# Performance work log

Hardware: AMD Instinct MI355X
Metric: run time of the kernel (lower is better)

## Reference

```python
import jax, jax.numpy as jnp
import numpy as np

B, T, D = 128, 80, 2048
H = 512          # visual_rnn_size; bidirectional output = 2H = 1024
K = 512          # visual_kernel_num
WS = (2, 3, 4, 5)
MAP_IN, MAP_OUT = 2 * H + len(WS) * K + D, 2048
EPS_BN = 1e-5


def _gru_dir(x, Wih, Whh, bih, bhh, reverse):
    """Single-direction PyTorch-convention GRU over [B,T,D] -> [B,T,H]."""
    Hh = Whh.shape[1]
    pre = jnp.einsum('btd,gd->btg', x, Wih) + bih  # [B,T,3H], gates (r,z,n)
    if reverse:
        pre = pre[:, ::-1]

    def step(h, p):
        gh = h @ Whh.T + bhh
        r = jax.nn.sigmoid(p[..., :Hh] + gh[..., :Hh])
        z = jax.nn.sigmoid(p[..., Hh:2 * Hh] + gh[..., Hh:2 * Hh])
        n = jnp.tanh(p[..., 2 * Hh:] + r * gh[..., 2 * Hh:])
        hn = (1.0 - z) * n + z * h
        return hn, hn

    h0 = jnp.zeros((x.shape[0], Hh), x.dtype)
    _, hs = jax.lax.scan(step, h0, jnp.swapaxes(pre, 0, 1))
    hs = jnp.swapaxes(hs, 0, 1)
    return hs[:, ::-1] if reverse else hs


def setup_inputs() -> dict:
    key = jax.random.key(0)
    ks = iter(jax.random.split(key, 40))
    f32 = jnp.float32

    videos = jax.random.normal(next(ks), (B, T, D), f32)
    videos_origin = jax.random.normal(next(ks), (B, D), f32)
    lengths = jax.random.randint(next(ks), (B,), 1, T + 1, jnp.int32)
    vidoes_mask = (jnp.arange(T)[None, :] < lengths[:, None]).astype(f32)
    gru_text_out = jax.random.normal(next(ks), (B, 1024), f32)

    def lin(k, fan_in, shape):
        return jax.random.normal(k, shape, f32) * (1.0 / np.sqrt(fan_in))

    inp = dict(videos=videos, videos_origin=videos_origin, lengths=lengths,
               vidoes_mask=vidoes_mask, gru_text_out=gru_text_out)
    # bidirectional GRU params (PyTorch layout: [3H, in])
    inp['Wih_f'] = lin(next(ks), D, (3 * H, D)); inp['Whh_f'] = lin(next(ks), H, (3 * H, H))
    inp['bih_f'] = jnp.zeros((3 * H,), f32);     inp['bhh_f'] = jnp.zeros((3 * H,), f32)
    inp['Wih_b'] = lin(next(ks), D, (3 * H, D)); inp['Whh_b'] = lin(next(ks), H, (3 * H, H))
    inp['bih_b'] = jnp.zeros((3 * H,), f32);     inp['bhh_b'] = jnp.zeros((3 * H,), f32)
    # attention layer
    inp['att_W1'] = lin(next(ks), 2 * H, (2 * H, 2 * H)); inp['att_b1'] = jnp.zeros((2 * H,), f32)
    inp['att_W2'] = lin(next(ks), 2 * H, (1, 2 * H));     inp['att_b2'] = jnp.zeros((1,), f32)
    # multi-window convs: kernel [K, 1, w, 2H]
    for w in WS:
        inp[f'conv_w{w}'] = lin(next(ks), w * 2 * H, (K, 1, w, 2 * H))
        inp[f'conv_b{w}'] = jnp.zeros((K,), f32)
    # visual mapping + BN
    inp['map_W'] = lin(next(ks), MAP_IN, (MAP_OUT, MAP_IN)); inp['map_b'] = jnp.zeros((MAP_OUT,), f32)
    inp['bn_gamma'] = jnp.ones((MAP_OUT,), f32); inp['bn_beta'] = jnp.zeros((MAP_OUT,), f32)
    return inp


def reference(videos, videos_origin, lengths, vidoes_mask, gru_text_out,
              Wih_f, Whh_f, bih_f, bhh_f, Wih_b, Whh_b, bih_b, bhh_b,
              att_W1, att_b1, att_W2, att_b2,
              conv_w2, conv_b2, conv_w3, conv_b3, conv_w4, conv_b4, conv_w5, conv_b5,
              map_W, map_b, bn_gamma, bn_beta):
    # bidirectional GRU -> [B,T,2H]
    gru = jnp.concatenate([
        _gru_dir(videos, Wih_f, Whh_f, bih_f, bhh_f, False),
        _gru_dir(videos, Wih_b, Whh_b, bih_b, bhh_b, True)], axis=-1)
    # attention (softmax over size-1 dim, as in the original)
    att = jax.nn.softmax(jnp.tanh(gru @ att_W1.T + att_b1) @ att_W2.T + att_b2, axis=-1)
    H2 = gru * att
    # ragged masked mean over valid frames (replaces per-sample python loop)
    len_f = lengths.astype(videos.dtype)
    mean_gru = jnp.sum(H2 * vidoes_mask[:, :, None], axis=1) / len_f[:, None]
    # multi-window CNN over masked sequence
    masked = (H2 * vidoes_mask[:, :, None])[:, None, :, :]  # [B,1,T,2H]
    convs = [(2, conv_w2, conv_b2), (3, conv_w3, conv_b3), (4, conv_w4, conv_b4), (5, conv_w5, conv_b5)]
    outs = []
    for (w, cw, cb) in convs:
        c = jax.lax.conv_general_dilated(masked, cw, (1, 1), [(w - 1, w - 1), (0, 0)],
                                         dimension_numbers=('NCHW', 'OIHW', 'NCHW'))
        c = jax.nn.relu(c + cb.reshape(1, -1, 1, 1))[..., 0]  # [B,K,T+w-1]
        outs.append(jnp.max(c, axis=2))
    con = jnp.concatenate(outs, axis=1)  # [B, 4K]
    # concate == 'full'
    feat = jnp.concatenate([mean_gru, con, videos_origin], axis=1) @ map_W.T + map_b
    # BatchNorm1d in eval mode (running_mean=0, running_var=1)
    feat = feat / jnp.sqrt(jnp.asarray(1.0 + EPS_BN, feat.dtype)) * bn_gamma + bn_beta
    # l2norm
    return feat / jnp.sqrt(jnp.sum(feat * feat, axis=1, keepdims=True))
```

## Files before the change

kernel.cpp:

```cpp
#include <hip/hip_runtime.h>
#include <hip/hip_bf16.h>


#define T_SEQ 80

typedef __attribute__((ext_vector_type(8))) short short8;
typedef __attribute__((ext_vector_type(4))) float floatx4;

__device__ __forceinline__ float bf2f(unsigned short s) {
    union { unsigned int u; float f; } c; c.u = ((unsigned int)s) << 16; return c.f;
}
__device__ __forceinline__ unsigned short f2bf(float f) {
    union { float f; unsigned int u; } c; c.f = f;
    unsigned int u = c.u;
    u += 0x7fffu + ((u >> 16) & 1u);
    return (unsigned short)(u >> 16);
}
__device__ __forceinline__ void gld16(const unsigned short* g, unsigned short* lds_uniform) {
    __builtin_amdgcn_global_load_lds(
        (const __attribute__((address_space(1))) void*)g,
        (__attribute__((address_space(3))) void*)lds_uniform, 16, 0, 0);
}
__device__ __forceinline__ void stage8_f32(const float* __restrict__ src, unsigned short* __restrict__ dst) {
    float4 a = *(const float4*)src;
    float4 b = *(const float4*)(src + 4);
    short8 v;
    v[0] = (short)f2bf(a.x); v[1] = (short)f2bf(a.y); v[2] = (short)f2bf(a.z); v[3] = (short)f2bf(a.w);
    v[4] = (short)f2bf(b.x); v[5] = (short)f2bf(b.y); v[6] = (short)f2bf(b.z); v[7] = (short)f2bf(b.w);
    *(short8*)dst = v;
}

__global__ __launch_bounds__(256) void k_f2b(
    const float* __restrict__ src, unsigned short* __restrict__ dst, int n8)
{
    int e = blockIdx.x * 256 + threadIdx.x;
    if (e >= n8) return;
    float4 a = ((const float4*)src)[e * 2];
    float4 b = ((const float4*)src)[e * 2 + 1];
    short8 v;
    v[0] = (short)f2bf(a.x); v[1] = (short)f2bf(a.y); v[2] = (short)f2bf(a.z); v[3] = (short)f2bf(a.w);
    v[4] = (short)f2bf(b.x); v[5] = (short)f2bf(b.y); v[6] = (short)f2bf(b.z); v[7] = (short)f2bf(b.w);
    *(short8*)(dst + e * 8) = v;
}

template<int AF32, int BF32, int OUTBF>
__global__ __launch_bounds__(256) void gemm_mfma(
    const void* __restrict__ Av, long a_base, int a_rpb, long a_bstride, int a_rstride,
    const void* __restrict__ B1v, const void* __restrict__ B2v,
    int n_split, int b_mod, long b_sa, long b_sb,
    const float* __restrict__ bias1, const float* __restrict__ bias2, int has_bias,
    void* __restrict__ Cout, long out_dsplit, long ldc,
    int kchunk, long zout)
{
    __shared__ __align__(16) unsigned short As[128 * 32];
    __shared__ __align__(16) unsigned short Bs[128 * 32];
    const int tid = threadIdx.x, wave = tid >> 6, lane = tid & 63;
    const int m0 = blockIdx.y * 128, n0 = blockIdx.x * 128;
    const long kbeg = (long)blockIdx.z * kchunk;

    const int c0 = wave * 64 + lane, c1 = 256 + c0;
    const int rA0 = c0 >> 2, pA0 = c0 & 3, rA1 = c1 >> 2, pA1 = c1 & 3;
    const int am0 = m0 + rA0, am1 = m0 + rA1;
    const long aoff0 = a_base + (long)(am0 / a_rpb) * a_bstride + (long)(am0 % a_rpb) * a_rstride + pA0 * 8 + kbeg;
    const long aoff1 = a_base + (long)(am1 / a_rpb) * a_bstride + (long)(am1 % a_rpb) * a_rstride + pA1 * 8 + kbeg;

    const int bn0 = n0 + rA0, bn1 = n0 + rA1;
    const int bd0 = (bn0 >= n_split), bd1 = (bn1 >= n_split);
    const int br0 = bn0 - (bd0 ? n_split : 0), br1 = bn1 - (bd1 ? n_split : 0);
    const long boff0 = (long)(br0 % b_mod) * b_sa + (long)(br0 / b_mod) * b_sb + pA0 * 8 + kbeg;
    const long boff1 = (long)(br1 % b_mod) * b_sa + (long)(br1 / b_mod) * b_sb + pA1 * 8 + kbeg;
    const void* Bp0 = bd0 ? B2v : B1v;
    const void* Bp1 = bd1 ? B2v : B1v;

    const int frow = lane & 15, fq = lane >> 4;
    const int wm = (wave >> 1) * 64, wn = (wave & 1) * 64;

    floatx4 acc[4][4];
    #pragma unroll
    for (int i = 0; i < 4; ++i)
        #pragma unroll
        for (int j = 0; j < 4; ++j) acc[i][j] = (floatx4)0.f;

    for (int k0 = 0; k0 < kchunk; k0 += 32) {
        if (AF32) {
            stage8_f32((const float*)Av + aoff0 + k0, As + c0 * 8);
            stage8_f32((const float*)Av + aoff1 + k0, As + c1 * 8);
        } else {
            gld16((const unsigned short*)Av + aoff0 + k0, As + (wave * 64) * 8);
            gld16((const unsigned short*)Av + aoff1 + k0, As + (256 + wave * 64) * 8);
        }
        if (BF32) {
            stage8_f32((const float*)Bp0 + boff0 + k0, Bs + c0 * 8);
            stage8_f32((const float*)Bp1 + boff1 + k0, Bs + c1 * 8);
        } else {
            gld16((const unsigned short*)Bp0 + boff0 + k0, Bs + (wave * 64) * 8);
            gld16((const unsigned short*)Bp1 + boff1 + k0, Bs + (256 + wave * 64) * 8);
        }
        __syncthreads();
        short8 af[4], bf[4];
        #pragma unroll
        for (int i = 0; i < 4; ++i) {
            af[i] = *(const short8*)&As[(wm + i * 16 + frow) * 32 + fq * 8];
            bf[i] = *(const short8*)&Bs[(wn + i * 16 + frow) * 32 + fq * 8];
        }
        #pragma unroll
        for (int mi = 0; mi < 4; ++mi)
            #pragma unroll
            for (int ni = 0; ni < 4; ++ni)
                acc[mi][ni] = __builtin_amdgcn_mfma_f32_16x16x32_bf16(af[mi], bf[ni], acc[mi][ni], 0, 0, 0);
        __syncthreads();
    }

    const long zoff = (long)blockIdx.z * zout;
    #pragma unroll
    for (int mi = 0; mi < 4; ++mi) {
        #pragma unroll
        for (int ni = 0; ni < 4; ++ni) {
            const int na = n0 + wn + ni * 16 + frow;
            const int dd = (na >= n_split);
            const int g  = na - (dd ? n_split : 0);
            float bv = has_bias ? (dd ? bias2 : bias1)[g] : 0.f;
            #pragma unroll
            for (int r = 0; r < 4; ++r) {
                const long gm = m0 + wm + mi * 16 + fq * 4 + r;
                const float v = acc[mi][ni][r] + bv;
                const long cidx = zoff + (dd ? out_dsplit : 0) + gm * ldc + g;
                if (OUTBF) ((unsigned short*)Cout)[cidx] = f2bf(v);
                else       ((float*)Cout)[cidx] = v;
            }
        }
    }
}

__global__ __launch_bounds__(256) void k_gru_scan(
    const unsigned short* __restrict__ pre,
    unsigned short* __restrict__ hbf2,
    unsigned short* __restrict__ Mp,
    unsigned int* __restrict__ counters,
    const float* __restrict__ Whh_f, const float* __restrict__ Whh_b,
    const float* __restrict__ bhh_f, const float* __restrict__ bhh_b)
{
    __shared__ __align__(16) unsigned short Wlds[96][520];

    const int tid = threadIdx.x, wave = tid >> 6, lane = tid & 63;
    const int bx = blockIdx.x;
    const int cc = bx >> 3, gid = bx & 7;
    const int d = gid >> 2, bb = gid & 3;
    const int c0 = cc * 32;
    const float* WhhD = d ? Whh_b : Whh_f;
    const float* bhhD = d ? bhh_b : bhh_f;

    for (int e = tid; e < 6144; e += 256) {
        const int r = e >> 6, p = e & 63;
        const int g = r >> 5, jp = r & 31;
        stage8_f32(WhhD + ((long)(g * 512 + c0 + jp)) * 512 + p * 8, &Wlds[r][p * 8]);
    }

    const int frow = lane & 15, fq = lane >> 4;
    const int wr = wave & 1, wc = wave >> 1;
    const int myc = c0 + wc * 16 + frow;
    const int rbase = wr * 16 + fq * 4;
    const long arow = (long)(bb * 32 + wr * 16 + frow) * 512 + fq * 8;
    const int even = ((frow & 1) == 0);
    const int cpair = myc & ~1;

    float bres[3];
    #pragma unroll
    for (int g = 0; g < 3; ++g) bres[g] = bhhD[g * 512 + myc];

    float hreg[4] = {0.f, 0.f, 0.f, 0.f};
    unsigned int* cnt = counters + gid * 64;

    float pv[3][4];
    {
        const int ti0 = d ? (T_SEQ - 1) : 0;
        #pragma unroll
        for (int q = 0; q < 4; ++q) {
            const unsigned short* pb = pre + (long)d * 15728640 + ((long)(bb * 32 + rbase + q) * T_SEQ + ti0) * 1536 + myc;
            pv[0][q] = bf2f(pb[0]); pv[1][q] = bf2f(pb[512]); pv[2][q] = bf2f(pb[1024]);
        }
    }

    __syncthreads();

    #pragma unroll 1
    for (int t = 0; t < T_SEQ; ++t) {
        const int ti = d ? (T_SEQ - 1 - t) : t;
        const unsigned short* hread = hbf2 + ((t & 1) * 2 + d) * 65536;

        short8 af[16];
        #pragma unroll
        for (int kk = 0; kk < 16; ++kk) {
            union { unsigned long long u[2]; short8 s; } cv;
            unsigned long long* p = (unsigned long long*)(hread + arow + kk * 32);
            cv.u[0] = __hip_atomic_load(p,     __ATOMIC_RELAXED, __HIP_MEMORY_SCOPE_AGENT);
            cv.u[1] = __hip_atomic_load(p + 1, __ATOMIC_RELAXED, __HIP_MEMORY_SCOPE_AGENT);
            af[kk] = cv.s;
        }

        floatx4 acc[3] = {(floatx4)0.f, (floatx4)0.f, (floatx4)0.f};
        #pragma unroll
        for (int kk = 0; kk < 16; ++kk) {
            #pragma unroll
            for (int g = 0; g < 3; ++g) {
                const short8 bfr = *(const short8*)&Wlds[g * 32 + wc * 16 + frow][kk * 32 + fq * 8];
                acc[g] = __builtin_amdgcn_mfma_f32_16x16x32_bf16(af[kk], bfr, acc[g], 0, 0, 0);
            }
        }

        unsigned long long hv4 = 0ull;
        #pragma unroll
        for (int q = 0; q < 4; ++q) {
            const float gr = acc[0][q] + bres[0];
            const float gz = acc[1][q] + bres[1];
            const float gn = acc[2][q] + bres[2];
            const float rr = 1.f / (1.f + expf(-(pv[0][q] + gr)));
            const float zz = 1.f / (1.f + expf(-(pv[1][q] + gz)));
            const float nn = tanhf(pv[2][q] + rr * gn);
            const float hnew = (1.f - zz) * nn + zz * hreg[q];
            hreg[q] = hnew;
            hv4 |= (unsigned long long)f2bf(hnew) << (16 * q);
        }

        const unsigned long long prt = __shfl_xor(hv4, 1, 64);
        unsigned short* hw = hbf2 + (((t + 1) & 1) * 2 + d) * 65536;
        #pragma unroll
        for (int s = 0; s < 2; ++s) {
            const int q = even ? s : (2 + s);
            const unsigned int lo = (unsigned int)((even ? hv4 : prt) >> (16 * q)) & 0xffffu;
            const unsigned int hi = (unsigned int)((even ? prt : hv4) >> (16 * q)) & 0xffffu;
            const unsigned int pk = lo | (hi << 16);
            const long rowg = bb * 32 + rbase + q;
            __hip_atomic_store((unsigned int*)(hw + rowg * 512 + cpair), pk,
                               __ATOMIC_RELAXED, __HIP_MEMORY_SCOPE_AGENT);
            *(unsigned int*)(Mp + rowg * 90112 + (long)(4 + ti) * 1024 + d * 512 + cpair) = pk;
        }

        if (t + 1 < T_SEQ) {
            const int tn = d ? (T_SEQ - 2 - t) : (t + 1);
            #pragma unroll
            for (int q = 0; q < 4; ++q) {
                const unsigned short* pb = pre + (long)d * 15728640 + ((long)(bb * 32 + rbase + q) * T_SEQ + tn) * 1536 + myc;
                pv[0][q] = bf2f(pb[0]); pv[1][q] = bf2f(pb[512]); pv[2][q] = bf2f(pb[1024]);
            }
        }

        __syncthreads();
        if (tid == 0) {
            __hip_atomic_fetch_add(cnt, 1u, __ATOMIC_RELAXED, __HIP_MEMORY_SCOPE_AGENT);
            const unsigned int target = (unsigned int)(t + 1) * 16u;
            while (__hip_atomic_load(cnt, __ATOMIC_RELAXED, __HIP_MEMORY_SCOPE_AGENT) < target)
                __builtin_amdgcn_s_sleep(1);
        }
        __syncthreads();
    }
}

__global__ __launch_bounds__(256) void k_mask_mean(
    unsigned short* __restrict__ Mp, const float* __restrict__ mask,
    const int* __restrict__ lengths, float* __restrict__ mean)
{
    const int b = blockIdx.y;
    const int c = blockIdx.x * 256 + threadIdx.x;
    float acc = 0.f;
    unsigned short* base = Mp + (long)b * 90112 + 4096 + c;
    for (int t = 0; t < T_SEQ; ++t) {
        float m = mask[b * T_SEQ + t];
        float v = bf2f(base[t * 1024]) * m;
        base[t * 1024] = f2bf(v);
        acc += v;
    }
    mean[b * 1024 + c] = acc / (float)lengths[b];
}

__global__ __launch_bounds__(256) void k_conv_epi(
    const unsigned short* __restrict__ D, const float* __restrict__ cb,
    float* __restrict__ con, int w, int widx)
{
    const int b  = blockIdx.y;
    const int kf = blockIdx.x * 256 + threadIdx.x;
    const int N  = w * 512;
    const unsigned short* Db = D + (long)b * T_SEQ * N;
    float mx = -1e30f;
    for (int t = 0; t < T_SEQ + w - 1; ++t) {
        float s = 0.f;
        for (int i = 0; i < w; ++i) {
            int tau = t - w + 1 + i;
            if (tau >= 0 && tau < T_SEQ) s += bf2f(Db[(long)tau * N + i * 512 + kf]);
        }
        mx = fmaxf(mx, s);
    }
    con[b * 2048 + widx * 512 + kf] = fmaxf(0.f, mx + cb[kf]);
}

__global__ __launch_bounds__(256) void k_gather(
    const float* __restrict__ mean, const float* __restrict__ con,
    const float* __restrict__ vo, unsigned short* __restrict__ fin)
{
    int e = blockIdx.x * 256 + threadIdx.x;
    int b = e / 5120, k = e - b * 5120;
    float v;
    if (k < 1024)      v = mean[b * 1024 + k];
    else if (k < 3072) v = con[b * 2048 + (k - 1024)];
    else               v = vo[b * 2048 + (k - 3072)];
    fin[e] = f2bf(v);
}

__global__ __launch_bounds__(256) void k_map_reduce(
    const float* __restrict__ part, const float* __restrict__ map_b,
    float* __restrict__ feat)
{
    int e = blockIdx.x * 256 + threadIdx.x;
    float s = map_b[e & 2047];
    #pragma unroll
    for (int z = 0; z < 8; ++z) s += part[(long)z * 262144 + e];
    feat[e] = s;
}

__global__ __launch_bounds__(256) void k_bn_norm(
    const float* __restrict__ feat, const float* __restrict__ gamma,
    const float* __restrict__ beta, float* __restrict__ out)
{
    const int b = blockIdx.x, tid = threadIdx.x;
    const float inv_c = 1.f / sqrtf(1.f + 1e-5f);
    float y[8]; float ss = 0.f;
    #pragma unroll
    for (int u = 0; u < 8; ++u) {
        int o = u * 256 + tid;
        float v = feat[b * 2048 + o] * inv_c * gamma[o] + beta[o];
        y[u] = v; ss += v * v;
    }
    #pragma unroll
    for (int off = 32; off >= 1; off >>= 1) ss += __shfl_down(ss, off, 64);
    __shared__ float rs[4];
    if ((tid & 63) == 0) rs[tid >> 6] = ss;
    __syncthreads();
    float rn = 1.f / sqrtf(rs[0] + rs[1] + rs[2] + rs[3]);
    #pragma unroll
    for (int u = 0; u < 8; ++u) {
        int o = u * 256 + tid;
        out[b * 2048 + o] = y[u] * rn;
    }
}

extern "C" void kernel_launch(void* const* d_in, const int* in_sizes, int n_in,
                              void* d_out, int out_size, void* d_ws, size_t ws_size,
                              hipStream_t stream)
{
    const float* videos  = (const float*)d_in[0];
    const float* vorigin = (const float*)d_in[1];
    const int*   lengths = (const int*)d_in[2];
    const float* mask    = (const float*)d_in[3];
    const float* Wih_f = (const float*)d_in[5];
    const float* Whh_f = (const float*)d_in[6];
    const float* bih_f = (const float*)d_in[7];
    const float* bhh_f = (const float*)d_in[8];
    const float* Wih_b = (const float*)d_in[9];
    const float* Whh_b = (const float*)d_in[10];
    const float* bih_b = (const float*)d_in[11];
    const float* bhh_b = (const float*)d_in[12];
    const float* cw[4] = { (const float*)d_in[17], (const float*)d_in[19],
                           (const float*)d_in[21], (const float*)d_in[23] };
    const float* cb[4] = { (const float*)d_in[18], (const float*)d_in[20],
                           (const float*)d_in[22], (const float*)d_in[24] };
    const float* map_W = (const float*)d_in[25];
    const float* map_b = (const float*)d_in[26];
    const float* gamma = (const float*)d_in[27];
    const float* beta  = (const float*)d_in[28];

    unsigned char* W = (unsigned char*)d_ws;
    unsigned short* pre    = (unsigned short*)W;
    unsigned short* Mp     = (unsigned short*)(W + 62914560);
    unsigned short* hbf2   = (unsigned short*)(W + 85983232);
    unsigned int*   counters = (unsigned int*)(W + 86507520);
    float*          mean   = (float*)(W + 88342528);
    float*          con    = (float*)(W + 88866816);
    unsigned short* fin    = (unsigned short*)(W + 89915392);
    float*          feat   = (float*)(W + 91226112);
    float*          part   = (float*)W;
    unsigned short* wih_bf  = (unsigned short*)(W + 62914560);
    unsigned short* cwbf    = (unsigned short*)(W + 57671680);
    unsigned short* mapw_bf = (unsigned short*)(W + 8388608);

    hipMemsetAsync(W + 85983232, 0, 524288 + 2048, stream);

    k_f2b<<<3072, 256, 0, stream>>>(Wih_f, wih_bf, 393216);
    k_f2b<<<3072, 256, 0, stream>>>(Wih_b, wih_bf + 3145728, 393216);

    gemm_mfma<1, 0, 1><<<dim3(24, 80, 1), 256, 0, stream>>>(
        videos, 0l, 10240, 0l, 2048,
        wih_bf, wih_bf + 3145728, 1536, 1536, 2048l, 0l,
        bih_f, bih_b, 1,
        pre, 15728640l, 1536l, 2048, 0l);

    {
        const unsigned short* prec = pre;
        void* args[] = { (void*)&prec, (void*)&hbf2, (void*)&Mp, (void*)&counters,
                         (void*)&Whh_f, (void*)&Whh_b, (void*)&bhh_f, (void*)&bhh_b };
        hipLaunchCooperativeKernel((const void*)k_gru_scan, dim3(128, 1, 1),
                                   dim3(256, 1, 1), args, 0, stream);
    }

    k_mask_mean<<<dim3(4, 128), 256, 0, stream>>>(Mp, mask, lengths, mean);

    for (int wi = 0; wi < 4; ++wi) {
        int ww = wi + 2;
        int N  = ww * 512;
        k_f2b<<<ww * 256, 256, 0, stream>>>(cw[wi], cwbf, ww * 65536);
        gemm_mfma<0, 0, 1><<<dim3(N / 128, 80, 1), 256, 0, stream>>>(
            Mp, 4096l, 80, 90112l, 1024,
            cwbf, nullptr, 1 << 30, 512, (long)(ww * 1024), 1024l,
            nullptr, nullptr, 0,
            pre, 0l, (long)N, 1024, 0l);
        k_conv_epi<<<dim3(2, 128), 256, 0, stream>>>(pre, cb[wi], con, ww, wi);
    }

    k_gather<<<2560, 256, 0, stream>>>(mean, con, vorigin, fin);

    k_f2b<<<5120, 256, 0, stream>>>(map_W, mapw_bf, 1310720);
    gemm_mfma<0, 0, 0><<<dim3(16, 1, 8), 256, 0, stream>>>(
        fin, 0l, 128, 0l, 5120,
        mapw_bf, nullptr, 1 << 30, 2048, 5120l, 0l,
        nullptr, nullptr, 0,
        part, 0l, 2048l, 640, 262144l);
    k_map_reduce<<<1024, 256, 0, stream>>>(part, map_b, feat);

    k_bn_norm<<<128, 256, 0, stream>>>(feat, gamma, beta, (float*)d_out);
}
```

Baseline: 1.696 ms.

## Use packed bf16 convert, M-major block raster, earlier barrier arrival in GRU scan

Replaces the software round-to-nearest fp32-to-bf16 conversion with the hardware v_cvt_pk_bf16_f32 instruction in the staging and conversion kernels. Remaps the GEMM grid to a 1D launch in which consecutive blocks walk the M dimension, so blocks running together share the same B (weight) tile in cache. In the GRU scan, each block signals the grid-wide step counter before prefetching the next timestep's preactivations, so that prefetch overlaps the wait for other blocks. The arrival happens before the prefetch loads complete, and the rounding of the hardware conversion may differ slightly for NaN and edge cases.

```diff
diff --git a/kernel.cpp b/kernel.cpp
--- a/kernel.cpp
+++ b/kernel.cpp
@@ -16,6 +16,11 @@
     u += 0x7fffu + ((u >> 16) & 1u);
     return (unsigned short)(u >> 16);
 }
+__device__ __forceinline__ unsigned int cvtpk(float lo, float hi) {
+    unsigned int r;
+    asm("v_cvt_pk_bf16_f32 %0, %1, %2" : "=v"(r) : "v"(lo), "v"(hi));
+    return r;
+}
 __device__ __forceinline__ void gld16(const unsigned short* g, unsigned short* lds_uniform) {
     __builtin_amdgcn_global_load_lds(
         (const __attribute__((address_space(1))) void*)g,
@@ -24,10 +29,10 @@
 __device__ __forceinline__ void stage8_f32(const float* __restrict__ src, unsigned short* __restrict__ dst) {
     float4 a = *(const float4*)src;
     float4 b = *(const float4*)(src + 4);
-    short8 v;
-    v[0] = (short)f2bf(a.x); v[1] = (short)f2bf(a.y); v[2] = (short)f2bf(a.z); v[3] = (short)f2bf(a.w);
-    v[4] = (short)f2bf(b.x); v[5] = (short)f2bf(b.y); v[6] = (short)f2bf(b.z); v[7] = (short)f2bf(b.w);
-    *(short8*)dst = v;
+    union { unsigned int u[4]; short8 s; } p;
+    p.u[0] = cvtpk(a.x, a.y); p.u[1] = cvtpk(a.z, a.w);
+    p.u[2] = cvtpk(b.x, b.y); p.u[3] = cvtpk(b.z, b.w);
+    *(short8*)dst = p.s;
 }
 
 __global__ __launch_bounds__(256) void k_f2b(
@@ -37,10 +42,10 @@
     if (e >= n8) return;
     float4 a = ((const float4*)src)[e * 2];
     float4 b = ((const float4*)src)[e * 2 + 1];
-    short8 v;
-    v[0] = (short)f2bf(a.x); v[1] = (short)f2bf(a.y); v[2] = (short)f2bf(a.z); v[3] = (short)f2bf(a.w);
-    v[4] = (short)f2bf(b.x); v[5] = (short)f2bf(b.y); v[6] = (short)f2bf(b.z); v[7] = (short)f2bf(b.w);
-    *(short8*)(dst + e * 8) = v;
+    union { unsigned int u[4]; short8 s; } p;
+    p.u[0] = cvtpk(a.x, a.y); p.u[1] = cvtpk(a.z, a.w);
+    p.u[2] = cvtpk(b.x, b.y); p.u[3] = cvtpk(b.z, b.w);
+    *(short8*)(dst + e * 8) = p.s;
 }
 
 template<int AF32, int BF32, int OUTBF>
@@ -50,12 +55,15 @@
     int n_split, int b_mod, long b_sa, long b_sb,
     const float* __restrict__ bias1, const float* __restrict__ bias2, int has_bias,
     void* __restrict__ Cout, long out_dsplit, long ldc,
-    int kchunk, long zout)
+    int kchunk, long zout, int m_rr)
 {
     __shared__ __align__(16) unsigned short As[128 * 32];
     __shared__ __align__(16) unsigned short Bs[128 * 32];
     const int tid = threadIdx.x, wave = tid >> 6, lane = tid & 63;
-    const int m0 = blockIdx.y * 128, n0 = blockIdx.x * 128;
+    int bxl, byl;
+    if (m_rr) { byl = (int)blockIdx.x % m_rr; bxl = (int)blockIdx.x / m_rr; }
+    else      { bxl = blockIdx.x; byl = blockIdx.y; }
+    const int m0 = byl * 128, n0 = bxl * 128;
     const long kbeg = (long)blockIdx.z * kchunk;
 
     const int c0 = wave * 64 + lane, c1 = 256 + c0;
@@ -236,6 +244,9 @@
             *(unsigned int*)(Mp + rowg * 90112 + (long)(4 + ti) * 1024 + d * 512 + cpair) = pk;
         }
 
+        __syncthreads();
+        if (tid == 0)
+            __hip_atomic_fetch_add(cnt, 1u, __ATOMIC_RELAXED, __HIP_MEMORY_SCOPE_AGENT);
         if (t + 1 < T_SEQ) {
             const int tn = d ? (T_SEQ - 2 - t) : (t + 1);
             #pragma unroll
@@ -244,10 +255,7 @@
                 pv[0][q] = bf2f(pb[0]); pv[1][q] = bf2f(pb[512]); pv[2][q] = bf2f(pb[1024]);
             }
         }
-
-        __syncthreads();
         if (tid == 0) {
-            __hip_atomic_fetch_add(cnt, 1u, __ATOMIC_RELAXED, __HIP_MEMORY_SCOPE_AGENT);
             const unsigned int target = (unsigned int)(t + 1) * 16u;
             while (__hip_atomic_load(cnt, __ATOMIC_RELAXED, __HIP_MEMORY_SCOPE_AGENT) < target)
                 __builtin_amdgcn_s_sleep(1);
@@ -387,11 +395,11 @@
     k_f2b<<<3072, 256, 0, stream>>>(Wih_f, wih_bf, 393216);
     k_f2b<<<3072, 256, 0, stream>>>(Wih_b, wih_bf + 3145728, 393216);
 
-    gemm_mfma<1, 0, 1><<<dim3(24, 80, 1), 256, 0, stream>>>(
+    gemm_mfma<1, 0, 1><<<dim3(24 * 80, 1, 1), 256, 0, stream>>>(
         videos, 0l, 10240, 0l, 2048,
         wih_bf, wih_bf + 3145728, 1536, 1536, 2048l, 0l,
         bih_f, bih_b, 1,
-        pre, 15728640l, 1536l, 2048, 0l);
+        pre, 15728640l, 1536l, 2048, 0l, 80);
 
     {
         const unsigned short* prec = pre;
@@ -407,11 +415,11 @@
         int ww = wi + 2;
         int N  = ww * 512;
         k_f2b<<<ww * 256, 256, 0, stream>>>(cw[wi], cwbf, ww * 65536);
-        gemm_mfma<0, 0, 1><<<dim3(N / 128, 80, 1), 256, 0, stream>>>(
+        gemm_mfma<0, 0, 1><<<dim3((N / 128) * 80, 1, 1), 256, 0, stream>>>(
             Mp, 4096l, 80, 90112l, 1024,
             cwbf, nullptr, 1 << 30, 512, (long)(ww * 1024), 1024l,
             nullptr, nullptr, 0,
-            pre, 0l, (long)N, 1024, 0l);
+            pre, 0l, (long)N, 1024, 0l, 80);
         k_conv_epi<<<dim3(2, 128), 256, 0, stream>>>(pre, cb[wi], con, ww, wi);
     }
 
@@ -422,7 +430,7 @@
         fin, 0l, 128, 0l, 5120,
         mapw_bf, nullptr, 1 << 30, 2048, 5120l, 0l,
         nullptr, nullptr, 0,
-        part, 0l, 2048l, 640, 262144l);
+        part, 0l, 2048l, 640, 262144l, 0);
     k_map_reduce<<<1024, 256, 0, stream>>>(part, map_b, feat);
 
     k_bn_norm<<<128, 256, 0, stream>>>(feat, gamma, beta, (float*)d_out);
```

New measurement: 1.616 ms. 1.05x faster.
